# Performance work log

Measured on AMD Instinct MI355X. Metric: run time of the kernel, lower is better.

Reference implementation:

```python
import jax, jax.numpy as jnp
import numpy as np

B, N, F_ = 4, 2048, 512
H = 8
D = F_ // H


def setup_inputs() -> dict:
    key = jax.random.key(0)
    ks = jax.random.split(key, 9)
    s = 1.0 / np.sqrt(F_)
    return {
        "x": jax.random.normal(ks[0], (B, N, F_), dtype=jnp.float32),
        "Wq": jax.random.normal(ks[1], (F_, F_), dtype=jnp.float32) * s,
        "bq": jax.random.normal(ks[2], (F_,), dtype=jnp.float32) * 0.01,
        "Wk": jax.random.normal(ks[3], (F_, F_), dtype=jnp.float32) * s,
        "bk": jax.random.normal(ks[4], (F_,), dtype=jnp.float32) * 0.01,
        "Wv": jax.random.normal(ks[5], (F_, F_), dtype=jnp.float32) * s,
        "bv": jax.random.normal(ks[6], (F_,), dtype=jnp.float32) * 0.01,
        "Wo": jax.random.normal(ks[7], (F_, F_), dtype=jnp.float32) * s,
        "bo": jax.random.normal(ks[8], (F_,), dtype=jnp.float32) * 0.01,
    }


def reference(x, Wq, bq, Wk, bk, Wv, bv, Wo, bo):
    b, n, f = x.shape
    h, d = H, f // H
    # projections -> [b, h, n, d]
    q = (x @ Wq + bq).reshape(b, n, h, d).transpose(0, 2, 1, 3)
    k = (x @ Wk + bk).reshape(b, n, h, d).transpose(0, 2, 1, 3)
    v = (x @ Wv + bv).reshape(b, n, h, d).transpose(0, 2, 1, 3)
    # NOTE: module scales by sqrt(feats), not sqrt(head_dim)
    sqrt_d = jnp.asarray(f, x.dtype) ** 0.5
    score = jax.nn.softmax(jnp.einsum('bhif,bhjf->bhij', q, k) / sqrt_d, axis=-1)
    attn = jnp.einsum('bhij,bhjf->bihf', score, v).reshape(b, n, f)
    return attn @ Wo + bo
```

## Files before the change

### kernel.cpp

```cpp
#include <hip/hip_runtime.h>


typedef _Float16 f16;
typedef _Float16 f16x2 __attribute__((ext_vector_type(2)));
typedef _Float16 f16x4 __attribute__((ext_vector_type(4)));
typedef _Float16 f16x8 __attribute__((ext_vector_type(8)));
typedef float f32x4 __attribute__((ext_vector_type(4)));

#define MFMA16(a, b, c) __builtin_amdgcn_mfma_f32_16x16x32_f16((a), (b), (c), 0, 0, 0)
#if __has_builtin(__builtin_amdgcn_exp2f)
#define EXP2(x) __builtin_amdgcn_exp2f(x)
#else
#define EXP2(x) exp2f(x)
#endif
#define GLLDS16(gp, lp)                                                    \
  __builtin_amdgcn_global_load_lds(                                        \
      (const __attribute__((address_space(1))) unsigned int*)(gp),         \
      (__attribute__((address_space(3))) unsigned int*)(lp), 16, 0, 0)

#define QSCALE 0.0637587f

__global__ __launch_bounds__(256) void k_cvt_x(const float* __restrict__ x,
                                               f16* __restrict__ xb, int n4) {
  int i = blockIdx.x * 256 + threadIdx.x;
  const int stride = gridDim.x * 256;
  const float4* xp = (const float4*)x;
  f16x4* op = (f16x4*)xb;
  for (; i < n4; i += stride) {
    float4 v = xp[i];
    f16x4 o = {(f16)v.x, (f16)v.y, (f16)v.z, (f16)v.w};
    op[i] = o;
  }
}

__global__ __launch_bounds__(256) void k_cvt_w(const float* __restrict__ Wq,
                                               const float* __restrict__ Wk,
                                               const float* __restrict__ Wv,
                                               const float* __restrict__ Wo,
                                               f16* __restrict__ wt) {
  const int w = blockIdx.y;
  const float* W = (w == 0) ? Wq : (w == 1) ? Wk : (w == 2) ? Wv : Wo;
  const int j0 = (blockIdx.x >> 4) * 32;
  const int k0 = (blockIdx.x & 15) * 32;
  __shared__ float tl[32][33];
  const int tx = threadIdx.x & 31, ty = threadIdx.x >> 5;
#pragma unroll
  for (int i = 0; i < 32; i += 8)
    tl[ty + i][tx] = W[(size_t)(k0 + ty + i) * 512 + j0 + tx];
  __syncthreads();
#pragma unroll
  for (int i = 0; i < 32; i += 8)
    wt[(size_t)w * 262144 + (size_t)(j0 + ty + i) * 512 + (k0 + tx)] =
        (f16)tl[tx][ty + i];
}

template <int BN, int MODE>
__global__ __launch_bounds__(256) void k_gemm(
    const f16* __restrict__ A, const f16* __restrict__ Wb3,
    const float* __restrict__ bias0, const float* __restrict__ bias1,
    const float* __restrict__ bias2, f16* __restrict__ oQ, f16* __restrict__ oK,
    f16* __restrict__ oV, float* __restrict__ oOut) {
  __shared__ __align__(16) f16 a_lds[128 * 64];
  __shared__ __align__(16) f16 b_lds[BN * 64];
  const int t = threadIdx.x;
  const int lane = t & 63, wid = t >> 6;
  const int l15 = lane & 15, l4 = lane >> 4;
  constexpr int MT = (BN == 128) ? 4 : 2;
  const int mbase = (BN == 128) ? (wid >> 1) * 64 : wid * 32;
  const int nbase = (BN == 128) ? (wid & 1) * 64 : 0;
  const int m0 = blockIdx.x * 128;
  const int by = blockIdx.y;
  const int wsel = (MODE == 0) ? (by >> 2) : 0;
  const int n0l = (MODE == 0) ? ((by & 3) * 128) : (by * (BN == 64 ? 64 : 128));
  const f16* Wt = Wb3 + (size_t)wsel * 262144;

  const int srow = t >> 3;
  const int sswz = ((t & 7) ^ (srow & 7)) * 8;
  const f16* Ag = A + (size_t)(m0 + srow) * 512 + sswz;
  const f16* Bg = Wt + (size_t)(n0l + srow) * 512 + sswz;

  f32x4 acc[MT][4];
  const f32x4 z4 = {0.f, 0.f, 0.f, 0.f};
#pragma unroll
  for (int i = 0; i < MT; i++)
#pragma unroll
    for (int j = 0; j < 4; j++) acc[i][j] = z4;

  for (int k0 = 0; k0 < 512; k0 += 64) {
#pragma unroll
    for (int i = 0; i < 4; i++)
      GLLDS16(Ag + (size_t)i * 16384 + k0, &a_lds[i * 2048 + wid * 512]);
#pragma unroll
    for (int i = 0; i < BN / 32; i++)
      GLLDS16(Bg + (size_t)i * 16384 + k0, &b_lds[i * 2048 + wid * 512]);
    __syncthreads();
#pragma unroll
    for (int ks = 0; ks < 2; ks++) {
      const int rs = ((ks * 4 + l4) ^ (l15 & 7)) * 8;
      f16x8 af[MT], bf[4];
#pragma unroll
      for (int mt = 0; mt < MT; mt++)
        af[mt] = *(const f16x8*)&a_lds[(mbase + mt * 16 + l15) * 64 + rs];
#pragma unroll
      for (int nt = 0; nt < 4; nt++)
        bf[nt] = *(const f16x8*)&b_lds[(nbase + nt * 16 + l15) * 64 + rs];
      __builtin_amdgcn_s_setprio(1);
#pragma unroll
      for (int mt = 0; mt < MT; mt++)
#pragma unroll
        for (int nt = 0; nt < 4; nt++)
          acc[mt][nt] = MFMA16(af[mt], bf[nt], acc[mt][nt]);
      __builtin_amdgcn_s_setprio(0);
    }
    __syncthreads();
  }

  if (MODE == 1) {
#pragma unroll
    for (int mt = 0; mt < MT; mt++)
#pragma unroll
      for (int nt = 0; nt < 4; nt++) {
        const int row = m0 + mbase + mt * 16 + l4 * 4;
        const int col = n0l + nbase + nt * 16 + l15;
        const float bv = bias0[col];
#pragma unroll
        for (int r = 0; r < 4; r++)
          oOut[(size_t)(row + r) * 512 + col] = acc[mt][nt][r] + bv;
      }
  } else {
#pragma unroll
    for (int mt = 0; mt < MT; mt++)
#pragma unroll
      for (int nt = 0; nt < 4; nt++) {
        const int colg = by * 128 + nbase + nt * 16 + l15;
        const int w = colg >> 9, jj = colg & 511;
        const int h = jj >> 6, d = jj & 63;
        const float* bp = (w == 0) ? bias0 : (w == 1) ? bias1 : bias2;
        const float bv = bp[jj];
        const float scl = (w == 0) ? QSCALE : 1.0f;
        const int rowg = m0 + mbase + mt * 16 + l4 * 4;
        const int b = rowg >> 11, nn = rowg & 2047;
        if (w == 2) {
          const size_t vb = ((size_t)(b * 8 + h) * 64 + d) * 2048 + nn;
#pragma unroll
          for (int r = 0; r < 4; r++)
            oV[vb + r] = (f16)(acc[mt][nt][r] + bv);
        } else {
          f16* op = (w == 0) ? oQ : oK;
          const size_t base = ((size_t)(b * 8 + h) * 2048 + nn) * 64 + d;
#pragma unroll
          for (int r = 0; r < 4; r++)
            op[base + (size_t)r * 64] = (f16)((acc[mt][nt][r] + bv) * scl);
        }
      }
  }
}

__global__ __launch_bounds__(256, 2) void k_attn(const f16* __restrict__ Q,
                                                 const f16* __restrict__ K,
                                                 const f16* __restrict__ Vt,
                                                 f16* __restrict__ CTX) {
  __shared__ __align__(16) f16 k_lds[3][4096];
  __shared__ __align__(16) f16 v_lds[3][4096];
  const int t = threadIdx.x, wid = t >> 6, lane = t & 63;
  const int l15 = lane & 15, l4 = lane >> 4;
  const int bid = blockIdx.x;
  const int bh = (bid & 7) * 4 + (bid >> 7);
  const int qb = (bid >> 3) & 15;
  const int q0 = qb * 128 + wid * 32;
  const size_t kvb = (size_t)bh * (2048 * 64);

  f16x8 qf[2][2];
#pragma unroll
  for (int g = 0; g < 2; g++)
#pragma unroll
    for (int ks = 0; ks < 2; ks++)
      qf[g][ks] = *(const f16x8*)&Q[kvb + (size_t)(q0 + g * 16 + l15) * 64 +
                                    ks * 32 + l4 * 8];

  f32x4 oa[2][4];
  f32x4 lacc[2];
  const f32x4 z4 = {0.f, 0.f, 0.f, 0.f};
#pragma unroll
  for (int g = 0; g < 2; g++) {
    lacc[g] = z4;
#pragma unroll
    for (int dt = 0; dt < 4; dt++) oa[g][dt] = z4;
  }
  const f16 one = (f16)1.0f;
  const f16x8 ones = {one, one, one, one, one, one, one, one};

  const int krow = wid * 8 + (lane >> 3);
  const int kswz = ((lane & 7) ^ (lane >> 3)) * 8;
  const int kperm = ((krow & 0x0C) << 1) | ((krow & 0x10) >> 2) | (krow & 3);
  const f16* Kg = K + kvb + (size_t)kperm * 64 + kswz;
  const f16* Vg = Vt + kvb + (size_t)krow * 2048 + kswz;

#pragma unroll
  for (int p = 0; p < 2; p++) {
    GLLDS16(Kg + p * 4096, &k_lds[p][wid * 512]);
    GLLDS16(Kg + p * 4096 + 2048, &k_lds[p][wid * 512 + 2048]);
    GLLDS16(Vg + p * 64, &v_lds[p][wid * 512]);
    GLLDS16(Vg + p * 64 + 32 * 2048, &v_lds[p][wid * 512 + 2048]);
  }
  __syncthreads();

  int cur = 0, stg = 2;
  for (int it = 0; it < 32; ++it) {
    if (it < 30) {
      const size_t kb = (size_t)(it + 2) * 4096;
      const size_t vb = (size_t)(it + 2) * 64;
      GLLDS16(Kg + kb, &k_lds[stg][wid * 512]);
      GLLDS16(Kg + kb + 2048, &k_lds[stg][wid * 512 + 2048]);
      GLLDS16(Vg + vb, &v_lds[stg][wid * 512]);
      GLLDS16(Vg + vb + 32 * 2048, &v_lds[stg][wid * 512 + 2048]);
    }

    f32x4 st[2][4];
#pragma unroll
    for (int g = 0; g < 2; g++)
#pragma unroll
      for (int w = 0; w < 4; w++) st[g][w] = z4;
    const f16* kl = &k_lds[cur][0];
#pragma unroll
    for (int ks = 0; ks < 2; ks++) {
      const int rs = ((ks * 4 + l4) ^ (l15 & 7)) * 8;
      f16x8 kf[4];
#pragma unroll
      for (int w = 0; w < 4; w++)
        kf[w] = *(const f16x8*)&kl[(w * 16 + l15) * 64 + rs];
      __builtin_amdgcn_s_setprio(1);
#pragma unroll
      for (int w = 0; w < 4; w++) {
        st[0][w] = MFMA16(kf[w], qf[0][ks], st[0][w]);
        st[1][w] = MFMA16(kf[w], qf[1][ks], st[1][w]);
      }
      __builtin_amdgcn_s_setprio(0);
    }

    f16x8 pa[2][2];
#pragma unroll
    for (int g = 0; g < 2; g++)
#pragma unroll
      for (int ks = 0; ks < 2; ks++) {
        f16x2 a0 = __builtin_bit_cast(
            f16x2, __builtin_amdgcn_cvt_pkrtz(EXP2(st[g][2 * ks][0]),
                                              EXP2(st[g][2 * ks][1])));
        f16x2 a1 = __builtin_bit_cast(
            f16x2, __builtin_amdgcn_cvt_pkrtz(EXP2(st[g][2 * ks][2]),
                                              EXP2(st[g][2 * ks][3])));
        f16x2 a2 = __builtin_bit_cast(
            f16x2, __builtin_amdgcn_cvt_pkrtz(EXP2(st[g][2 * ks + 1][0]),
                                              EXP2(st[g][2 * ks + 1][1])));
        f16x2 a3 = __builtin_bit_cast(
            f16x2, __builtin_amdgcn_cvt_pkrtz(EXP2(st[g][2 * ks + 1][2]),
                                              EXP2(st[g][2 * ks + 1][3])));
        f16x8 p;
        p[0] = a0[0]; p[1] = a0[1]; p[2] = a1[0]; p[3] = a1[1];
        p[4] = a2[0]; p[5] = a2[1]; p[6] = a3[0]; p[7] = a3[1];
        pa[g][ks] = p;
      }

    const f16* vl = &v_lds[cur][0];
#pragma unroll
    for (int ks = 0; ks < 2; ks++) {
      __builtin_amdgcn_s_setprio(1);
      lacc[0] = MFMA16(pa[0][ks], ones, lacc[0]);
      lacc[1] = MFMA16(pa[1][ks], ones, lacc[1]);
#pragma unroll
      for (int dt = 0; dt < 4; dt++) {
        const f16x8 vf = *(const f16x8*)&vl[(dt * 16 + l15) * 64 +
                                            ((ks * 4 + l4) ^ (l15 & 7)) * 8];
        oa[0][dt] = MFMA16(pa[0][ks], vf, oa[0][dt]);
        oa[1][dt] = MFMA16(pa[1][ks], vf, oa[1][dt]);
      }
      __builtin_amdgcn_s_setprio(0);
    }

    if (it < 31) {
      if (it < 30)
        asm volatile("s_waitcnt vmcnt(4)" ::: "memory");
      else
        asm volatile("s_waitcnt vmcnt(0)" ::: "memory");
      __builtin_amdgcn_s_barrier();
      __builtin_amdgcn_sched_barrier(0);
    }
    cur = (cur == 2) ? 0 : cur + 1;
    stg = (stg == 2) ? 0 : stg + 1;
  }

  const int b = bh >> 3, h = bh & 7;
#pragma unroll
  for (int g = 0; g < 2; g++)
#pragma unroll
    for (int r = 0; r < 4; r++) {
      const float inv = 1.0f / lacc[g][r];
      const int qrow = q0 + g * 16 + l4 * 4 + r;
#pragma unroll
      for (int dt = 0; dt < 4; dt++)
        CTX[(size_t)(b * 2048 + qrow) * 512 + h * 64 + dt * 16 + l15] =
            (f16)(oa[g][dt][r] * inv);
    }
}

extern "C" void kernel_launch(void* const* d_in, const int* in_sizes, int n_in,
                              void* d_out, int out_size, void* d_ws,
                              size_t ws_size, hipStream_t stream) {
  const float* x = (const float*)d_in[0];
  const float* Wq = (const float*)d_in[1];
  const float* bq = (const float*)d_in[2];
  const float* Wk = (const float*)d_in[3];
  const float* bk = (const float*)d_in[4];
  const float* Wv = (const float*)d_in[5];
  const float* bv = (const float*)d_in[6];
  const float* Wo = (const float*)d_in[7];
  const float* bo = (const float*)d_in[8];
  float* out = (float*)d_out;
  char* ws = (char*)d_ws;

  f16* xb = (f16*)(ws);
  f16* wt = (f16*)(ws + (size_t)(8u << 20));
  f16* Qb = (f16*)(ws + (size_t)(10u << 20));
  f16* Kb = (f16*)(ws + (size_t)(18u << 20));
  f16* Vt = (f16*)(ws + (size_t)(26u << 20));
  f16* CX = (f16*)(ws + (size_t)(34u << 20));

  k_cvt_x<<<dim3(2048), dim3(256), 0, stream>>>(x, xb, 1048576);
  k_cvt_w<<<dim3(256, 4), dim3(256), 0, stream>>>(Wq, Wk, Wv, Wo, wt);
  k_gemm<128, 0><<<dim3(64, 12), dim3(256), 0, stream>>>(
      xb, wt, bq, bk, bv, Qb, Kb, Vt, nullptr);
  k_attn<<<dim3(512), dim3(256), 0, stream>>>(Qb, Kb, Vt, CX);
  k_gemm<64, 1><<<dim3(64, 8), dim3(256), 0, stream>>>(
      CX, wt + (size_t)3 * 262144, bo, nullptr, nullptr, nullptr, nullptr,
      nullptr, out);
}
```

Measured before the change: 84.66 us.

## Load V fragments directly from global into registers; double-buffer only K in LDS

```diff
diff --git a/kernel.cpp b/kernel.cpp
--- a/kernel.cpp
+++ b/kernel.cpp
@@ -160,8 +160,7 @@
                                                  const f16* __restrict__ K,
                                                  const f16* __restrict__ Vt,
                                                  f16* __restrict__ CTX) {
-  __shared__ __align__(16) f16 k_lds[3][4096];
-  __shared__ __align__(16) f16 v_lds[3][4096];
+  __shared__ __align__(16) f16 k_lds[2][4096];
   const int t = threadIdx.x, wid = t >> 6, lane = t & 63;
   const int l15 = lane & 15, l4 = lane >> 4;
   const int bid = blockIdx.x;
@@ -194,26 +193,29 @@
   const int kswz = ((lane & 7) ^ (lane >> 3)) * 8;
   const int kperm = ((krow & 0x0C) << 1) | ((krow & 0x10) >> 2) | (krow & 3);
   const f16* Kg = K + kvb + (size_t)kperm * 64 + kswz;
-  const f16* Vg = Vt + kvb + (size_t)krow * 2048 + kswz;
-
-#pragma unroll
-  for (int p = 0; p < 2; p++) {
-    GLLDS16(Kg + p * 4096, &k_lds[p][wid * 512]);
-    GLLDS16(Kg + p * 4096 + 2048, &k_lds[p][wid * 512 + 2048]);
-    GLLDS16(Vg + p * 64, &v_lds[p][wid * 512]);
-    GLLDS16(Vg + p * 64 + 32 * 2048, &v_lds[p][wid * 512 + 2048]);
-  }
+
+  const f16* Vr[4];
+#pragma unroll
+  for (int dt = 0; dt < 4; dt++)
+    Vr[dt] = Vt + kvb + (size_t)(dt * 16 + l15) * 2048 + l4 * 8;
+
+  GLLDS16(Kg, &k_lds[0][wid * 512]);
+  GLLDS16(Kg + 2048, &k_lds[0][wid * 512 + 2048]);
   __syncthreads();
 
-  int cur = 0, stg = 2;
+  int cur = 0;
   for (int it = 0; it < 32; ++it) {
-    if (it < 30) {
-      const size_t kb = (size_t)(it + 2) * 4096;
-      const size_t vb = (size_t)(it + 2) * 64;
-      GLLDS16(Kg + kb, &k_lds[stg][wid * 512]);
-      GLLDS16(Kg + kb + 2048, &k_lds[stg][wid * 512 + 2048]);
-      GLLDS16(Vg + vb, &v_lds[stg][wid * 512]);
-      GLLDS16(Vg + vb + 32 * 2048, &v_lds[stg][wid * 512 + 2048]);
+    f16x8 vg[2][4];
+#pragma unroll
+    for (int ks = 0; ks < 2; ks++)
+#pragma unroll
+      for (int dt = 0; dt < 4; dt++)
+        vg[ks][dt] = *(const f16x8*)&Vr[dt][it * 64 + ks * 32];
+
+    if (it < 31) {
+      const size_t kb = (size_t)(it + 1) * 4096;
+      GLLDS16(Kg + kb, &k_lds[cur ^ 1][wid * 512]);
+      GLLDS16(Kg + kb + 2048, &k_lds[cur ^ 1][wid * 512 + 2048]);
     }
 
     f32x4 st[2][4];
@@ -261,7 +263,6 @@
         pa[g][ks] = p;
       }
 
-    const f16* vl = &v_lds[cur][0];
 #pragma unroll
     for (int ks = 0; ks < 2; ks++) {
       __builtin_amdgcn_s_setprio(1);
@@ -269,24 +270,13 @@
       lacc[1] = MFMA16(pa[1][ks], ones, lacc[1]);
 #pragma unroll
       for (int dt = 0; dt < 4; dt++) {
-        const f16x8 vf = *(const f16x8*)&vl[(dt * 16 + l15) * 64 +
-                                            ((ks * 4 + l4) ^ (l15 & 7)) * 8];
-        oa[0][dt] = MFMA16(pa[0][ks], vf, oa[0][dt]);
-        oa[1][dt] = MFMA16(pa[1][ks], vf, oa[1][dt]);
+        oa[0][dt] = MFMA16(pa[0][ks], vg[ks][dt], oa[0][dt]);
+        oa[1][dt] = MFMA16(pa[1][ks], vg[ks][dt], oa[1][dt]);
       }
       __builtin_amdgcn_s_setprio(0);
     }
-
-    if (it < 31) {
-      if (it < 30)
-        asm volatile("s_waitcnt vmcnt(4)" ::: "memory");
-      else
-        asm volatile("s_waitcnt vmcnt(0)" ::: "memory");
-      __builtin_amdgcn_s_barrier();
-      __builtin_amdgcn_sched_barrier(0);
-    }
-    cur = (cur == 2) ? 0 : cur + 1;
-    stg = (stg == 2) ? 0 : stg + 1;
+    __syncthreads();
+    cur ^= 1;
   }
 
   const int b = bh >> 3, h = bh & 7;
```

After: 108.4 us. 28.1% more time.

## Software-pipeline attention loop so next tile's QK overlaps current exp and PV

Applied to the files above, without the earlier changes.

```diff
diff --git a/kernel.cpp b/kernel.cpp
--- a/kernel.cpp
+++ b/kernel.cpp
@@ -196,32 +196,11 @@
   const f16* Kg = K + kvb + (size_t)kperm * 64 + kswz;
   const f16* Vg = Vt + kvb + (size_t)krow * 2048 + kswz;
 
-#pragma unroll
-  for (int p = 0; p < 2; p++) {
-    GLLDS16(Kg + p * 4096, &k_lds[p][wid * 512]);
-    GLLDS16(Kg + p * 4096 + 2048, &k_lds[p][wid * 512 + 2048]);
-    GLLDS16(Vg + p * 64, &v_lds[p][wid * 512]);
-    GLLDS16(Vg + p * 64 + 32 * 2048, &v_lds[p][wid * 512 + 2048]);
-  }
-  __syncthreads();
-
-  int cur = 0, stg = 2;
-  for (int it = 0; it < 32; ++it) {
-    if (it < 30) {
-      const size_t kb = (size_t)(it + 2) * 4096;
-      const size_t vb = (size_t)(it + 2) * 64;
-      GLLDS16(Kg + kb, &k_lds[stg][wid * 512]);
-      GLLDS16(Kg + kb + 2048, &k_lds[stg][wid * 512 + 2048]);
-      GLLDS16(Vg + vb, &v_lds[stg][wid * 512]);
-      GLLDS16(Vg + vb + 32 * 2048, &v_lds[stg][wid * 512 + 2048]);
-    }
-
-    f32x4 st[2][4];
+  auto QK = [&](const f16* kl, f32x4(&st)[2][4]) {
 #pragma unroll
     for (int g = 0; g < 2; g++)
 #pragma unroll
       for (int w = 0; w < 4; w++) st[g][w] = z4;
-    const f16* kl = &k_lds[cur][0];
 #pragma unroll
     for (int ks = 0; ks < 2; ks++) {
       const int rs = ((ks * 4 + l4) ^ (l15 & 7)) * 8;
@@ -229,16 +208,14 @@
 #pragma unroll
       for (int w = 0; w < 4; w++)
         kf[w] = *(const f16x8*)&kl[(w * 16 + l15) * 64 + rs];
-      __builtin_amdgcn_s_setprio(1);
 #pragma unroll
       for (int w = 0; w < 4; w++) {
         st[0][w] = MFMA16(kf[w], qf[0][ks], st[0][w]);
         st[1][w] = MFMA16(kf[w], qf[1][ks], st[1][w]);
       }
-      __builtin_amdgcn_s_setprio(0);
-    }
-
-    f16x8 pa[2][2];
+    }
+  };
+  auto EXPPACK = [&](f32x4(&st)[2][4], f16x8(&pa)[2][2]) {
 #pragma unroll
     for (int g = 0; g < 2; g++)
 #pragma unroll
@@ -260,11 +237,10 @@
         p[4] = a2[0]; p[5] = a2[1]; p[6] = a3[0]; p[7] = a3[1];
         pa[g][ks] = p;
       }
-
-    const f16* vl = &v_lds[cur][0];
+  };
+  auto PV = [&](const f16* vl, f16x8(&pa)[2][2]) {
 #pragma unroll
     for (int ks = 0; ks < 2; ks++) {
-      __builtin_amdgcn_s_setprio(1);
       lacc[0] = MFMA16(pa[0][ks], ones, lacc[0]);
       lacc[1] = MFMA16(pa[1][ks], ones, lacc[1]);
 #pragma unroll
@@ -274,19 +250,47 @@
         oa[0][dt] = MFMA16(pa[0][ks], vf, oa[0][dt]);
         oa[1][dt] = MFMA16(pa[1][ks], vf, oa[1][dt]);
       }
-      __builtin_amdgcn_s_setprio(0);
-    }
-
+    }
+  };
+  auto STAGE = [&](int tile, int buf) {
+    const size_t kb = (size_t)tile * 4096;
+    const size_t vb = (size_t)tile * 64;
+    f16* kd = &k_lds[0][0] + buf * 4096 + wid * 512;
+    f16* vd = &v_lds[0][0] + buf * 4096 + wid * 512;
+    GLLDS16(Kg + kb, kd);
+    GLLDS16(Kg + kb + 2048, kd + 2048);
+    GLLDS16(Vg + vb, vd);
+    GLLDS16(Vg + vb + 32 * 2048, vd + 2048);
+  };
+  auto body = [&](int it, int cur, f32x4(&stC)[2][4], f32x4(&stN)[2][4]) {
+    const int nxt = (cur < 2) ? cur + 1 : 0;
+    const int stg = (nxt < 2) ? nxt + 1 : 0;
+    if (it < 30) STAGE(it + 2, stg);
+    __builtin_amdgcn_s_setprio(1);
+    f16x8 pa[2][2];
+    EXPPACK(stC, pa);
+    if (it < 31) QK(&k_lds[0][0] + nxt * 4096, stN);
+    PV(&v_lds[0][0] + cur * 4096, pa);
+    __builtin_amdgcn_s_setprio(0);
     if (it < 31) {
-      if (it < 30)
-        asm volatile("s_waitcnt vmcnt(4)" ::: "memory");
-      else
-        asm volatile("s_waitcnt vmcnt(0)" ::: "memory");
+      asm volatile("s_waitcnt vmcnt(0)" ::: "memory");
       __builtin_amdgcn_s_barrier();
       __builtin_amdgcn_sched_barrier(0);
     }
-    cur = (cur == 2) ? 0 : cur + 1;
-    stg = (stg == 2) ? 0 : stg + 1;
+  };
+
+  STAGE(0, 0);
+  STAGE(1, 1);
+  __syncthreads();
+  f32x4 stA[2][4], stB[2][4];
+  QK(&k_lds[0][0], stA);
+
+  int cur = 0;
+  for (int it = 0; it < 32; it += 2) {
+    body(it, cur, stA, stB);
+    cur = (cur < 2) ? cur + 1 : 0;
+    body(it + 1, cur, stB, stA);
+    cur = (cur < 2) ? cur + 1 : 0;
   }
 
   const int b = bh >> 3, h = bh & 7;
```

Measured after the change: 85.04 us. No clear change (+0.4%).
